# Performance work log

Measured on AMD Instinct MI355X. Metric: run time of the kernel, lower is better.

The kernel has to match this reference:

```python
import jax, jax.numpy as jnp
import numpy as np

D = 2            # qudit dimension (init kwarg)
INDEX = (0, 1, 2)  # qudits the Hadamard acts on (init kwarg)
N = 8192         # state dimension D**L, L = 13
B = 4096         # batch of state vectors


def _hadamard_matrix():
    # For D=2: omega = exp(2j*pi/2) = -1, so M is exactly real.
    return jnp.array([[1.0, 1.0], [1.0, -1.0]], dtype=jnp.float32) * (2.0 ** -0.5)


def setup_inputs() -> dict:
    key = jax.random.key(0)
    x = jax.random.normal(key, (N, B), dtype=jnp.float32)
    M = _hadamard_matrix()
    return {"x": x, "M": M}


def reference(x, M):
    # L qudits of dimension D; static from shapes
    L = int(round(np.log(x.shape[0]) / np.log(D)))
    batch = x.shape[1]
    # reshape state to one axis per qudit plus trailing batch axis
    t = x.reshape((D,) * L + (batch,))
    # apply the small DxD gate along each targeted qudit axis
    # (mathematically identical to kron(I,...,M,...,I) @ x)
    for ax in INDEX:
        t = jnp.moveaxis(jnp.tensordot(M, t, axes=([1], [ax])), 0, ax)
    return t.reshape(x.shape)
```

## Files before the change

### kernel.cpp

```cpp
#include <hip/hip_runtime.h>


typedef float f32x4 __attribute__((ext_vector_type(4)));

__global__ __launch_bounds__(256) void hgate8_kernel(const float* __restrict__ x,
                                                     float* __restrict__ y) {
    const unsigned t = blockIdx.x * 256u + threadIdx.x;
    const unsigned c = t & 511u;
    const unsigned g = t >> 9;

    const size_t base0 = (size_t)g * 1024u + c;
    const size_t base1 = base0 + 512u;
    const size_t jstr  = 1048576u;

    const f32x4* __restrict__ xv = (const f32x4*)x;
    f32x4* __restrict__ yv = (f32x4*)y;

    f32x4 u[8], w[8];
#pragma unroll
    for (int j = 0; j < 8; ++j) u[j] = xv[base0 + j * jstr];
#pragma unroll
    for (int j = 0; j < 8; ++j) w[j] = xv[base1 + j * jstr];

    const float s = 0.35355339059327379f;

#define FWHT8_STORE(v, base)                                            \
    {                                                                   \
        f32x4 a0 = v[0] + v[1], a1 = v[0] - v[1];                       \
        f32x4 a2 = v[2] + v[3], a3 = v[2] - v[3];                       \
        f32x4 a4 = v[4] + v[5], a5 = v[4] - v[5];                       \
        f32x4 a6 = v[6] + v[7], a7 = v[6] - v[7];                       \
        f32x4 b0 = a0 + a2, b2 = a0 - a2;                               \
        f32x4 b1 = a1 + a3, b3 = a1 - a3;                               \
        f32x4 b4 = a4 + a6, b6 = a4 - a6;                               \
        f32x4 b5 = a5 + a7, b7 = a5 - a7;                               \
        __builtin_nontemporal_store((b0 + b4) * s, &yv[base + 0 * jstr]); \
        __builtin_nontemporal_store((b1 + b5) * s, &yv[base + 1 * jstr]); \
        __builtin_nontemporal_store((b2 + b6) * s, &yv[base + 2 * jstr]); \
        __builtin_nontemporal_store((b3 + b7) * s, &yv[base + 3 * jstr]); \
        __builtin_nontemporal_store((b0 - b4) * s, &yv[base + 4 * jstr]); \
        __builtin_nontemporal_store((b1 - b5) * s, &yv[base + 5 * jstr]); \
        __builtin_nontemporal_store((b2 - b6) * s, &yv[base + 6 * jstr]); \
        __builtin_nontemporal_store((b3 - b7) * s, &yv[base + 7 * jstr]); \
    }

    FWHT8_STORE(u, base0)
    FWHT8_STORE(w, base1)
#undef FWHT8_STORE
}

extern "C" void kernel_launch(void* const* d_in, const int* in_sizes, int n_in,
                              void* d_out, int out_size, void* d_ws, size_t ws_size,
                              hipStream_t stream) {
    const float* x = (const float*)d_in[0];
    float* y = (float*)d_out;

    hgate8_kernel<<<2048, 256, 0, stream>>>(x, y);
}
```

Measured before the change: 50.05 us.

## Halve per-thread work, rotate slab access order per block, drop nontemporal stores

```diff
diff --git a/kernel.cpp b/kernel.cpp
--- a/kernel.cpp
+++ b/kernel.cpp
@@ -5,48 +5,64 @@
 
 __global__ __launch_bounds__(256) void hgate8_kernel(const float* __restrict__ x,
                                                      float* __restrict__ y) {
-    const unsigned t = blockIdx.x * 256u + threadIdx.x;
-    const unsigned c = t & 511u;
-    const unsigned g = t >> 9;
+    const unsigned t   = blockIdx.x * 256u + threadIdx.x;
+    const unsigned col = t & 1023u;
+    const unsigned g   = t >> 10;
 
-    const size_t base0 = (size_t)g * 1024u + c;
-    const size_t base1 = base0 + 512u;
-    const size_t jstr  = 1048576u;
+    const size_t base = (size_t)g * 1024u + col;
+    const size_t jstr = 1048576u;
 
     const f32x4* __restrict__ xv = (const f32x4*)x;
     f32x4* __restrict__ yv = (f32x4*)y;
 
-    f32x4 u[8], w[8];
-#pragma unroll
-    for (int j = 0; j < 8; ++j) u[j] = xv[base0 + j * jstr];
-#pragma unroll
-    for (int j = 0; j < 8; ++j) w[j] = xv[base1 + j * jstr];
+    f32x4 v0, v1, v2, v3, v4, v5, v6, v7;
+
+    const unsigned rot = blockIdx.x & 7u;
+
+#define LD(j) v##j = xv[base + j * jstr];
+#define LOADS(a,b,c,d,e,f,g2,h) { LD(a) LD(b) LD(c) LD(d) LD(e) LD(f) LD(g2) LD(h) }
+    switch (rot) {
+        case 0: LOADS(0,1,2,3,4,5,6,7) break;
+        case 1: LOADS(1,2,3,4,5,6,7,0) break;
+        case 2: LOADS(2,3,4,5,6,7,0,1) break;
+        case 3: LOADS(3,4,5,6,7,0,1,2) break;
+        case 4: LOADS(4,5,6,7,0,1,2,3) break;
+        case 5: LOADS(5,6,7,0,1,2,3,4) break;
+        case 6: LOADS(6,7,0,1,2,3,4,5) break;
+        default: LOADS(7,0,1,2,3,4,5,6) break;
+    }
+#undef LOADS
+#undef LD
+
+    f32x4 a0 = v0 + v1, a1 = v0 - v1;
+    f32x4 a2 = v2 + v3, a3 = v2 - v3;
+    f32x4 a4 = v4 + v5, a5 = v4 - v5;
+    f32x4 a6 = v6 + v7, a7 = v6 - v7;
+    f32x4 b0 = a0 + a2, b2 = a0 - a2;
+    f32x4 b1 = a1 + a3, b3 = a1 - a3;
+    f32x4 b4 = a4 + a6, b6 = a4 - a6;
+    f32x4 b5 = a5 + a7, b7 = a5 - a7;
 
     const float s = 0.35355339059327379f;
+    f32x4 r0 = (b0 + b4) * s, r4 = (b0 - b4) * s;
+    f32x4 r1 = (b1 + b5) * s, r5 = (b1 - b5) * s;
+    f32x4 r2 = (b2 + b6) * s, r6 = (b2 - b6) * s;
+    f32x4 r3 = (b3 + b7) * s, r7 = (b3 - b7) * s;
 
-#define FWHT8_STORE(v, base)                                            \
-    {                                                                   \
-        f32x4 a0 = v[0] + v[1], a1 = v[0] - v[1];                       \
-        f32x4 a2 = v[2] + v[3], a3 = v[2] - v[3];                       \
-        f32x4 a4 = v[4] + v[5], a5 = v[4] - v[5];                       \
-        f32x4 a6 = v[6] + v[7], a7 = v[6] - v[7];                       \
-        f32x4 b0 = a0 + a2, b2 = a0 - a2;                               \
-        f32x4 b1 = a1 + a3, b3 = a1 - a3;                               \
-        f32x4 b4 = a4 + a6, b6 = a4 - a6;                               \
-        f32x4 b5 = a5 + a7, b7 = a5 - a7;                               \
-        __builtin_nontemporal_store((b0 + b4) * s, &yv[base + 0 * jstr]); \
-        __builtin_nontemporal_store((b1 + b5) * s, &yv[base + 1 * jstr]); \
-        __builtin_nontemporal_store((b2 + b6) * s, &yv[base + 2 * jstr]); \
-        __builtin_nontemporal_store((b3 + b7) * s, &yv[base + 3 * jstr]); \
-        __builtin_nontemporal_store((b0 - b4) * s, &yv[base + 4 * jstr]); \
-        __builtin_nontemporal_store((b1 - b5) * s, &yv[base + 5 * jstr]); \
-        __builtin_nontemporal_store((b2 - b6) * s, &yv[base + 6 * jstr]); \
-        __builtin_nontemporal_store((b3 - b7) * s, &yv[base + 7 * jstr]); \
+#define ST(j) yv[base + j * jstr] = r##j;
+#define STORES(a,b,c,d,e,f,g2,h) { ST(a) ST(b) ST(c) ST(d) ST(e) ST(f) ST(g2) ST(h) }
+    switch (rot) {
+        case 0: STORES(0,1,2,3,4,5,6,7) break;
+        case 1: STORES(1,2,3,4,5,6,7,0) break;
+        case 2: STORES(2,3,4,5,6,7,0,1) break;
+        case 3: STORES(3,4,5,6,7,0,1,2) break;
+        case 4: STORES(4,5,6,7,0,1,2,3) break;
+        case 5: STORES(5,6,7,0,1,2,3,4) break;
+        case 6: STORES(6,7,0,1,2,3,4,5) break;
+        default: STORES(7,0,1,2,3,4,5,6) break;
     }
-
-    FWHT8_STORE(u, base0)
-    FWHT8_STORE(w, base1)
-#undef FWHT8_STORE
+#undef STORES
+#undef ST
 }
 
 extern "C" void kernel_launch(void* const* d_in, const int* in_sizes, int n_in,
@@ -55,5 +71,5 @@
     const float* x = (const float*)d_in[0];
     float* y = (float*)d_out;
 
-    hgate8_kernel<<<2048, 256, 0, stream>>>(x, y);
+    hgate8_kernel<<<4096, 256, 0, stream>>>(x, y);
 }
```

Measured after the change: 46.25 us. -7.6%, faster.
